# Optimization experiments

Hardware: AMD Instinct MI355X
Metric: run time of the kernel (lower is better)

Reference implementation:

```python
import jax, jax.numpy as jnp
import numpy as np

N_NODES = 100000
N_EDGES = 1600000
IN_FEATS = 256
OUT_FEATS = 128


def setup_inputs() -> dict:
    key = jax.random.key(0)
    k1, k2, k3, k4 = jax.random.split(key, 4)
    feat = jax.random.normal(k1, (N_NODES, IN_FEATS), dtype=jnp.float32)
    # Glorot-uniform-like weight
    limit = np.sqrt(6.0 / (IN_FEATS + OUT_FEATS)).astype(np.float32)
    weight = jax.random.uniform(k2, (IN_FEATS, OUT_FEATS), dtype=jnp.float32,
                                minval=-limit, maxval=limit)
    bias = jnp.zeros((OUT_FEATS,), dtype=jnp.float32)
    src = jax.random.randint(k3, (N_EDGES,), 0, N_NODES, dtype=jnp.int32)
    dst = jax.random.randint(k4, (N_EDGES,), 0, N_NODES, dtype=jnp.int32)
    return {"feat": feat, "weight": weight, "bias": bias, "src": src, "dst": dst}


def reference(feat, weight, bias, src, dst):
    n = feat.shape[0]
    # in-degree per node (edges point src -> dst), clipped to >= 1
    deg = jax.ops.segment_sum(jnp.ones_like(dst, dtype=feat.dtype), dst,
                              num_segments=n)
    norm = jnp.clip(deg, 1.0, None) ** -0.5          # [N]
    norm = norm[:, None]                             # [N, 1]
    h = feat * norm                                  # src-side normalization
    # in_feats > out_feats: project first, then aggregate (cheaper messages)
    h = h @ weight                                   # [N, out]
    agg = jax.ops.segment_sum(h[src], dst, num_segments=n)  # sparse sum-aggregate
    rst = agg * norm + bias                          # dst-side norm + bias
    return rst
```

## Files before the change

kernel.cpp:

```cpp
#include <hip/hip_runtime.h>
#include <hip/hip_bf16.h>

#define IN_F 256
#define OUT_F 128
#define BSH 7
#define BNODES 128
#define MAXBUCK 1024
#define BIN1A_BLOCKS 256
#define BIN1B_BLOCKS 256
#define GEMM_BLOCKS 256
#define BM 32

typedef short bf16x8 __attribute__((ext_vector_type(8)));
typedef float f32x4 __attribute__((ext_vector_type(4)));
typedef unsigned short us8 __attribute__((ext_vector_type(8)));

__device__ __forceinline__ unsigned short f2bf(float x) {
    union { __hip_bfloat16 b; unsigned short u; } cv;
    cv.b = __float2bfloat16(x);
    return cv.u;
}
__device__ inline float bf2f(unsigned short x) {
    union { unsigned u; float f; } v; v.u = ((unsigned)x) << 16;
    return v.f;
}

__device__ __forceinline__ void gload_lds16(const void* g, void* l) {
    __builtin_amdgcn_global_load_lds(
        (const __attribute__((address_space(1))) unsigned int*)g,
        (__attribute__((address_space(3))) unsigned int*)l,
        16, 0, 0);
}

__global__ __launch_bounds__(256) void prep_kernel(const float* __restrict__ W,
                                                   unsigned short* __restrict__ Wt,
                                                   const int* __restrict__ dst,
                                                   int* __restrict__ bhist,
                                                   int* __restrict__ perbhist,
                                                   int n_edges, int nbuck) {
    if ((int)blockIdx.x < BIN1A_BLOCKS) {
        __shared__ int hist[MAXBUCK];
        const int tid = threadIdx.x;
        const int chunk = (n_edges + BIN1A_BLOCKS - 1) / BIN1A_BLOCKS;
        const int lo = blockIdx.x * chunk;
        const int hi = min(lo + chunk, n_edges);

        for (int i = tid; i < MAXBUCK; i += 256) hist[i] = 0;
        __syncthreads();
        for (int e = lo + tid; e < hi; e += 256)
            atomicAdd(&hist[dst[e] >> BSH], 1);
        __syncthreads();
        int* myrow = perbhist + (size_t)blockIdx.x * MAXBUCK;
        for (int i = tid; i < nbuck; i += 256) {
            int c = hist[i];
            myrow[i] = c;
            if (c) atomicAdd(&bhist[i], c);
        }
    } else {
        int n = blockIdx.x - BIN1A_BLOCKS;
        int k = threadIdx.x;
        Wt[n * IN_F + k] = f2bf(W[k * OUT_F + n]);
    }
}

__global__ __launch_bounds__(1024) void bin1b_kernel(const int* __restrict__ src,
                                                     const int* __restrict__ dst,
                                                     const int* __restrict__ bhist,
                                                     const int* __restrict__ perbhist,
                                                     int* __restrict__ gcur0,
                                                     unsigned* __restrict__ ebuf,
                                                     int n_edges, int nbuck) {
    __shared__ int scanv[MAXBUCK];
    __shared__ int hist[MAXBUCK];
    __shared__ int lbase[MAXBUCK];
    const int tid = threadIdx.x;
    const int chunk = (n_edges + BIN1B_BLOCKS - 1) / BIN1B_BLOCKS;
    const int lo = blockIdx.x * chunk;
    const int hi = min(lo + chunk, n_edges);

    int own = (tid < nbuck) ? bhist[tid] : 0;
    scanv[tid] = own;
    __syncthreads();
    #pragma unroll
    for (int off = 1; off < MAXBUCK; off <<= 1) {
        int t = (tid >= off) ? scanv[tid - off] : 0;
        __syncthreads();
        scanv[tid] += t;
        __syncthreads();
    }
    int bstart_t = scanv[tid] - own;
    __syncthreads();
    scanv[tid] = bstart_t;
    __syncthreads();

    if (tid < nbuck) {
        int c = perbhist[(size_t)blockIdx.x * MAXBUCK + tid];
        lbase[tid] = (c > 0) ? (scanv[tid] + atomicAdd(&gcur0[tid], c)) : 0;
        hist[tid] = 0;
    }
    __syncthreads();
    for (int e = lo + tid; e < hi; e += 1024) {
        int d = dst[e];
        int bkt = d >> BSH;
        int off = atomicAdd(&hist[bkt], 1);
        ebuf[lbase[bkt] + off] = ((unsigned)src[e] << BSH) | (unsigned)(d & (BNODES - 1));
    }
}

__global__ __launch_bounds__(1024) void gemm_mfma(const float* __restrict__ feat,
                                                  const unsigned short* __restrict__ Wt,
                                                  unsigned short* __restrict__ h,
                                                  int n_nodes) {
    __shared__ float As[3][BM * IN_F];

    const int tid  = threadIdx.x;
    const int wave = tid >> 6;
    const int lane = tid & 63;
    const int q    = lane >> 4;
    const int rr   = lane & 15;
    const int rowgrp = wave & 1;
    const int colgrp = wave >> 1;

    const int ntiles = (n_nodes + BM - 1) / BM;
    const int nit = ((int)blockIdx.x < ntiles)
                  ? ((ntiles - (int)blockIdx.x + GEMM_BLOCKS - 1) / GEMM_BLOCKS) : 0;

    const int brow = colgrp * 16 + rr;

    bf16x8 bq[8];
    #pragma unroll
    for (int k0 = 0; k0 < 8; ++k0)
        bq[k0] = *reinterpret_cast<const bf16x8*>(
            Wt + (size_t)brow * IN_F + (k0 * 4 + q) * 8);

    #pragma unroll
    for (int pb = 0; pb < 2; ++pb) {
        if (pb < nit) {
            const int R0 = ((int)blockIdx.x + pb * GEMM_BLOCKS) * BM;
            #pragma unroll
            for (int ii = 0; ii < 2; ++ii) {
                int r  = ii * 16 + wave;
                int rg = R0 + r; if (rg >= n_nodes) rg = n_nodes - 1;
                gload_lds16(feat + (size_t)rg * IN_F + ((lane ^ (r & 7)) * 4),
                            &As[pb][r * IN_F]);
            }
        }
    }

    const int arow = rowgrp * 16 + rr;

    int t = (int)blockIdx.x;
    for (int i = 0; i < nit; ++i, t += GEMM_BLOCKS) {
        if (nit < 4)          asm volatile("s_waitcnt vmcnt(0)" ::: "memory");
        else if (i == 0)      asm volatile("s_waitcnt vmcnt(2)" ::: "memory");
        else if (i == 1)      asm volatile("s_waitcnt vmcnt(6)" ::: "memory");
        else if (i < nit - 1) asm volatile("s_waitcnt vmcnt(10)" ::: "memory");
        else                  asm volatile("s_waitcnt vmcnt(8)" ::: "memory");
        __builtin_amdgcn_s_barrier();

        if (i + 2 < nit) {
            const int R0n = (t + 2 * GEMM_BLOCKS) * BM;
            float* dbuf = As[(i + 2) % 3];
            #pragma unroll
            for (int ii = 0; ii < 2; ++ii) {
                int r  = ii * 16 + wave;
                int rg = R0n + r; if (rg >= n_nodes) rg = n_nodes - 1;
                gload_lds16(feat + (size_t)rg * IN_F + ((lane ^ (r & 7)) * 4),
                            &dbuf[r * IN_F]);
            }
        }

        f32x4 acc = (f32x4){0.f, 0.f, 0.f, 0.f};
        const f32x4* ap = reinterpret_cast<const f32x4*>(&As[i % 3][arow * IN_F]);
        #pragma unroll
        for (int k0 = 0; k0 < 8; ++k0) {
            f32x4 a0 = ap[(k0 * 8 + 2 * q)     ^ (rr & 7)];
            f32x4 a1 = ap[(k0 * 8 + 2 * q + 1) ^ (rr & 7)];
            bf16x8 afr;
            afr[0] = (short)f2bf(a0[0]);
            afr[1] = (short)f2bf(a0[1]);
            afr[2] = (short)f2bf(a0[2]);
            afr[3] = (short)f2bf(a0[3]);
            afr[4] = (short)f2bf(a1[0]);
            afr[5] = (short)f2bf(a1[1]);
            afr[6] = (short)f2bf(a1[2]);
            afr[7] = (short)f2bf(a1[3]);
            acc = __builtin_amdgcn_mfma_f32_16x16x32_bf16(afr, bq[k0], acc, 0, 0, 0);
        }

        const int orow0 = t * BM + rowgrp * 16 + q * 4;
        const int col   = colgrp * 16 + rr;
        #pragma unroll
        for (int j = 0; j < 4; ++j)
            h[(size_t)(orow0 + j) * OUT_F + col] = f2bf(acc[j]);
    }
}

__global__ __launch_bounds__(256) void bin2_kernel(const unsigned* __restrict__ ebuf,
                                                   const int* __restrict__ bhist,
                                                   int* __restrict__ rstart,
                                                   float* __restrict__ norm,
                                                   int* __restrict__ eidx,
                                                   int n_nodes, int nbuck) {
    __shared__ int bs[MAXBUCK];
    __shared__ int lcnt[BNODES];
    __shared__ int lex[BNODES];
    __shared__ int sh[256];
    const int tid = threadIdx.x;
    const int node0 = blockIdx.x << BSH;

    {
        int v[4], s = 0;
        #pragma unroll
        for (int j = 0; j < 4; ++j) {
            int idx = tid * 4 + j;
            v[j] = (idx < nbuck) ? bhist[idx] : 0;
            s += v[j];
        }
        sh[tid] = s;
        __syncthreads();
        #pragma unroll
        for (int off = 1; off < 256; off <<= 1) {
            int t = (tid >= off) ? sh[tid - off] : 0;
            __syncthreads();
            sh[tid] += t;
            __syncthreads();
        }
        int ex = sh[tid] - s;
        #pragma unroll
        for (int j = 0; j < 4; ++j) {
            bs[tid * 4 + j] = ex;
            ex += v[j];
        }
    }
    __syncthreads();

    const int e0 = bs[blockIdx.x];
    const int e1 = e0 + bhist[blockIdx.x];

    if (tid < BNODES) lcnt[tid] = 0;
    __syncthreads();
    for (int e = e0 + tid; e < e1; e += 256)
        atomicAdd(&lcnt[ebuf[e] & (BNODES - 1)], 1);
    __syncthreads();

    int own = (tid < BNODES) ? lcnt[tid] : 0;
    if (tid < BNODES) lex[tid] = own;
    __syncthreads();
    #pragma unroll
    for (int off = 1; off < BNODES; off <<= 1) {
        int t = (tid >= off && tid < BNODES) ? lex[tid - off] : 0;
        __syncthreads();
        if (tid < BNODES) lex[tid] += t;
        __syncthreads();
    }
    if (tid < BNODES) {
        int ex = lex[tid] - own;
        lex[tid] = ex;
        int g = node0 + tid;
        if (g <= n_nodes) rstart[g] = e0 + ex;
        if (g < n_nodes) {
            float d = (float)own;
            if (d < 1.0f) d = 1.0f;
            norm[g] = 1.0f / sqrtf(d);
        }
        lcnt[tid] = 0;
    }
    __syncthreads();

    for (int e = e0 + tid; e < e1; e += 256) {
        unsigned pk = ebuf[e];
        int dl = pk & (BNODES - 1);
        int pos = atomicAdd(&lcnt[dl], 1);
        eidx[e0 + lex[dl] + pos] = (int)(pk >> BSH);
    }
}

__global__ __launch_bounds__(256) void agg_kernel(const unsigned short* __restrict__ h,
                                                  const int* __restrict__ eidx,
                                                  const int* __restrict__ rstart,
                                                  const float* __restrict__ norm,
                                                  const float* __restrict__ bias,
                                                  float* __restrict__ out,
                                                  int n_nodes) {
    const int wave = threadIdx.x >> 6;
    const int lane = threadIdx.x & 63;
    const int grp  = lane >> 4;
    const int gl   = lane & 15;
    const int node = blockIdx.x * 4 + wave;
    if (node >= n_nodes) return;

    const int start = rstart[node];
    const int cnt   = rstart[node + 1] - start;
    const unsigned short* __restrict__ hb = h + gl * 8;

    float acc[8] = {0.f, 0.f, 0.f, 0.f, 0.f, 0.f, 0.f, 0.f};

    for (int base = 0; base < cnt; base += 64) {
        const int rem = min(64, cnt - base);
        int   ev = (lane < rem) ? eidx[start + base + lane] : 0;
        float nv = (lane < rem) ? norm[ev] : 0.f;

        int j = 0;
        for (; j + 16 <= rem; j += 16) {
            int   s0 = __shfl(ev, j + grp);
            int   s1 = __shfl(ev, j + grp + 4);
            int   s2 = __shfl(ev, j + grp + 8);
            int   s3 = __shfl(ev, j + grp + 12);
            float n0 = __shfl(nv, j + grp);
            float n1 = __shfl(nv, j + grp + 4);
            float n2 = __shfl(nv, j + grp + 8);
            float n3 = __shfl(nv, j + grp + 12);
            us8 v0 = *reinterpret_cast<const us8*>(hb + (size_t)s0 * OUT_F);
            us8 v1 = *reinterpret_cast<const us8*>(hb + (size_t)s1 * OUT_F);
            us8 v2 = *reinterpret_cast<const us8*>(hb + (size_t)s2 * OUT_F);
            us8 v3 = *reinterpret_cast<const us8*>(hb + (size_t)s3 * OUT_F);
            #pragma unroll
            for (int qq = 0; qq < 8; ++qq) {
                acc[qq] += bf2f(v0[qq]) * n0 + bf2f(v1[qq]) * n1
                         + bf2f(v2[qq]) * n2 + bf2f(v3[qq]) * n3;
            }
        }
        for (; j < rem; j += 4) {
            int   je = j + grp;
            int   jc = min(je, rem - 1);
            int   s  = __shfl(ev, jc);
            float nm = __shfl(nv, jc);
            if (je >= rem) nm = 0.f;
            us8 v = *reinterpret_cast<const us8*>(hb + (size_t)s * OUT_F);
            #pragma unroll
            for (int qq = 0; qq < 8; ++qq)
                acc[qq] += bf2f(v[qq]) * nm;
        }
    }

    #pragma unroll
    for (int qq = 0; qq < 8; ++qq) {
        acc[qq] += __shfl_xor(acc[qq], 16);
        acc[qq] += __shfl_xor(acc[qq], 32);
    }

    if (grp == 0) {
        const float nd = norm[node];
        const float4 b0 = *reinterpret_cast<const float4*>(bias + gl * 8);
        const float4 b1 = *reinterpret_cast<const float4*>(bias + gl * 8 + 4);
        float4 r0, r1;
        r0.x = acc[0] * nd + b0.x;
        r0.y = acc[1] * nd + b0.y;
        r0.z = acc[2] * nd + b0.z;
        r0.w = acc[3] * nd + b0.w;
        r1.x = acc[4] * nd + b1.x;
        r1.y = acc[5] * nd + b1.y;
        r1.z = acc[6] * nd + b1.z;
        r1.w = acc[7] * nd + b1.w;
        float* o = out + (size_t)node * OUT_F + gl * 8;
        *reinterpret_cast<float4*>(o)     = r0;
        *reinterpret_cast<float4*>(o + 4) = r1;
    }
}

extern "C" void kernel_launch(void* const* d_in, const int* in_sizes, int n_in,
                              void* d_out, int out_size, void* d_ws, size_t ws_size,
                              hipStream_t stream) {
    const float* feat   = (const float*)d_in[0];
    const float* weight = (const float*)d_in[1];
    const float* bias   = (const float*)d_in[2];
    const int*   src    = (const int*)d_in[3];
    const int*   dst    = (const int*)d_in[4];
    float* out = (float*)d_out;

    const int n_nodes = in_sizes[0] / IN_F;
    const int n_edges = in_sizes[3];
    const int nbuck   = (n_nodes + BNODES - 1) >> BSH;

    char* ws = (char*)d_ws;
    size_t off = 0;
    auto alloc = [&](size_t bytes) {
        char* p = ws + off;
        off += (bytes + 15) & ~(size_t)15;
        return p;
    };
    unsigned short* h  = (unsigned short*)alloc((size_t)(n_nodes + BM) * OUT_F * 2);
    float* norm        = (float*)alloc((size_t)n_nodes * 4);
    int*   rstart      = (int*)alloc(((size_t)n_nodes + 1) * 4);
    int*   bhist       = (int*)alloc(2 * MAXBUCK * 4);
    int*   gcur0       = bhist + MAXBUCK;
    int*   perbhist    = (int*)alloc((size_t)BIN1A_BLOCKS * MAXBUCK * 4);
    unsigned short* Wt = (unsigned short*)alloc((size_t)OUT_F * IN_F * 2);
    unsigned* ebuf     = (unsigned*)alloc((size_t)n_edges * 4);
    int*   eidx        = (int*)alloc((size_t)n_edges * 4);

    hipMemsetAsync(bhist, 0, 2 * MAXBUCK * sizeof(int), stream);
    prep_kernel<<<BIN1A_BLOCKS + OUT_F, 256, 0, stream>>>(weight, Wt, dst, bhist,
                                                          perbhist, n_edges, nbuck);
    gemm_mfma<<<GEMM_BLOCKS, 1024, 0, stream>>>(feat, Wt, h, n_nodes);
    bin1b_kernel<<<BIN1B_BLOCKS, 1024, 0, stream>>>(src, dst, bhist, perbhist,
                                                    gcur0, ebuf, n_edges, nbuck);
    bin2_kernel<<<nbuck, 256, 0, stream>>>(ebuf, bhist, rstart, norm, eidx,
                                           n_nodes, nbuck);
    agg_kernel<<<(n_nodes + 3) / 4, 256, 0, stream>>>(h, eidx, rstart, norm, bias, out, n_nodes);
}
```

Measured before the change: 144.7 us.

## Merge GEMM and edge binning into one launch with double-buffered GEMM

Combines the bf16 MFMA projection kernel and the second edge-binning pass into one heterogeneous launch, where the first blocks do binning and the rest do GEMM, so the two independent stages can run at the same time on the GPU. It drops one kernel launch and lets memory-bound scatter work share the machine with the GEMM. The GEMM pipeline goes from a triple-buffered LDS scheme with hand-tuned vmcnt waits to a double buffer with __syncthreads, because the shared 64KB LDS allocation only fits two tiles. This may expose more load latency per tile, and the large static LDS now also applies to the binning blocks, limiting how many blocks fit per CU.

```diff
diff --git a/kernel.cpp b/kernel.cpp
--- a/kernel.cpp
+++ b/kernel.cpp
@@ -63,136 +63,130 @@
     }
 }
 
-__global__ __launch_bounds__(1024) void bin1b_kernel(const int* __restrict__ src,
-                                                     const int* __restrict__ dst,
-                                                     const int* __restrict__ bhist,
-                                                     const int* __restrict__ perbhist,
-                                                     int* __restrict__ gcur0,
-                                                     unsigned* __restrict__ ebuf,
-                                                     int n_edges, int nbuck) {
-    __shared__ int scanv[MAXBUCK];
-    __shared__ int hist[MAXBUCK];
-    __shared__ int lbase[MAXBUCK];
-    const int tid = threadIdx.x;
-    const int chunk = (n_edges + BIN1B_BLOCKS - 1) / BIN1B_BLOCKS;
-    const int lo = blockIdx.x * chunk;
-    const int hi = min(lo + chunk, n_edges);
-
-    int own = (tid < nbuck) ? bhist[tid] : 0;
-    scanv[tid] = own;
-    __syncthreads();
-    #pragma unroll
-    for (int off = 1; off < MAXBUCK; off <<= 1) {
-        int t = (tid >= off) ? scanv[tid - off] : 0;
-        __syncthreads();
-        scanv[tid] += t;
-        __syncthreads();
-    }
-    int bstart_t = scanv[tid] - own;
-    __syncthreads();
-    scanv[tid] = bstart_t;
-    __syncthreads();
-
-    if (tid < nbuck) {
-        int c = perbhist[(size_t)blockIdx.x * MAXBUCK + tid];
-        lbase[tid] = (c > 0) ? (scanv[tid] + atomicAdd(&gcur0[tid], c)) : 0;
-        hist[tid] = 0;
-    }
-    __syncthreads();
-    for (int e = lo + tid; e < hi; e += 1024) {
-        int d = dst[e];
-        int bkt = d >> BSH;
-        int off = atomicAdd(&hist[bkt], 1);
-        ebuf[lbase[bkt] + off] = ((unsigned)src[e] << BSH) | (unsigned)(d & (BNODES - 1));
-    }
-}
-
-__global__ __launch_bounds__(1024) void gemm_mfma(const float* __restrict__ feat,
-                                                  const unsigned short* __restrict__ Wt,
-                                                  unsigned short* __restrict__ h,
-                                                  int n_nodes) {
-    __shared__ float As[3][BM * IN_F];
-
-    const int tid  = threadIdx.x;
-    const int wave = tid >> 6;
-    const int lane = tid & 63;
-    const int q    = lane >> 4;
-    const int rr   = lane & 15;
-    const int rowgrp = wave & 1;
-    const int colgrp = wave >> 1;
-
-    const int ntiles = (n_nodes + BM - 1) / BM;
-    const int nit = ((int)blockIdx.x < ntiles)
-                  ? ((ntiles - (int)blockIdx.x + GEMM_BLOCKS - 1) / GEMM_BLOCKS) : 0;
-
-    const int brow = colgrp * 16 + rr;
-
-    bf16x8 bq[8];
-    #pragma unroll
-    for (int k0 = 0; k0 < 8; ++k0)
-        bq[k0] = *reinterpret_cast<const bf16x8*>(
-            Wt + (size_t)brow * IN_F + (k0 * 4 + q) * 8);
-
-    #pragma unroll
-    for (int pb = 0; pb < 2; ++pb) {
-        if (pb < nit) {
-            const int R0 = ((int)blockIdx.x + pb * GEMM_BLOCKS) * BM;
+__global__ __launch_bounds__(1024, 8) void gemm_bin_kernel(
+        const float* __restrict__ feat, const unsigned short* __restrict__ Wt,
+        unsigned short* __restrict__ h, int n_nodes,
+        const int* __restrict__ src, const int* __restrict__ dst,
+        const int* __restrict__ bhist, const int* __restrict__ perbhist,
+        int* __restrict__ gcur0, unsigned* __restrict__ ebuf,
+        int n_edges, int nbuck) {
+
+    __shared__ __align__(16) char smem[65536];
+
+    if ((int)blockIdx.x < BIN1B_BLOCKS) {
+        int* scanv = (int*)smem;
+        int* hist  = scanv + MAXBUCK;
+        int* lbase = hist + MAXBUCK;
+        const int tid = threadIdx.x;
+        const int chunk = (n_edges + BIN1B_BLOCKS - 1) / BIN1B_BLOCKS;
+        const int lo = blockIdx.x * chunk;
+        const int hi = min(lo + chunk, n_edges);
+
+        int own = (tid < nbuck) ? bhist[tid] : 0;
+        scanv[tid] = own;
+        __syncthreads();
+        #pragma unroll
+        for (int off = 1; off < MAXBUCK; off <<= 1) {
+            int t = (tid >= off) ? scanv[tid - off] : 0;
+            __syncthreads();
+            scanv[tid] += t;
+            __syncthreads();
+        }
+        int bstart_t = scanv[tid] - own;
+        __syncthreads();
+        scanv[tid] = bstart_t;
+        __syncthreads();
+
+        if (tid < nbuck) {
+            int c = perbhist[(size_t)blockIdx.x * MAXBUCK + tid];
+            lbase[tid] = (c > 0) ? (scanv[tid] + atomicAdd(&gcur0[tid], c)) : 0;
+            hist[tid] = 0;
+        }
+        __syncthreads();
+        for (int e = lo + tid; e < hi; e += 1024) {
+            int d = dst[e];
+            int bkt = d >> BSH;
+            int off = atomicAdd(&hist[bkt], 1);
+            ebuf[lbase[bkt] + off] = ((unsigned)src[e] << BSH) | (unsigned)(d & (BNODES - 1));
+        }
+    } else {
+        float (*As)[BM * IN_F] = (float (*)[BM * IN_F])smem;
+
+        const int tid  = threadIdx.x;
+        const int wave = tid >> 6;
+        const int lane = tid & 63;
+        const int q    = lane >> 4;
+        const int rr   = lane & 15;
+        const int rowgrp = wave & 1;
+        const int colgrp = wave >> 1;
+        const int gb   = (int)blockIdx.x - BIN1B_BLOCKS;
+
+        const int ntiles = (n_nodes + BM - 1) / BM;
+        const int nit = (gb < ntiles)
+                      ? ((ntiles - gb + GEMM_BLOCKS - 1) / GEMM_BLOCKS) : 0;
+
+        const int brow = colgrp * 16 + rr;
+
+        bf16x8 bq[8];
+        #pragma unroll
+        for (int k0 = 0; k0 < 8; ++k0)
+            bq[k0] = *reinterpret_cast<const bf16x8*>(
+                Wt + (size_t)brow * IN_F + (k0 * 4 + q) * 8);
+
+        if (0 < nit) {
+            const int R0 = gb * BM;
             #pragma unroll
             for (int ii = 0; ii < 2; ++ii) {
                 int r  = ii * 16 + wave;
                 int rg = R0 + r; if (rg >= n_nodes) rg = n_nodes - 1;
                 gload_lds16(feat + (size_t)rg * IN_F + ((lane ^ (r & 7)) * 4),
-                            &As[pb][r * IN_F]);
+                            &As[0][r * IN_F]);
             }
         }
-    }
-
-    const int arow = rowgrp * 16 + rr;
-
-    int t = (int)blockIdx.x;
-    for (int i = 0; i < nit; ++i, t += GEMM_BLOCKS) {
-        if (nit < 4)          asm volatile("s_waitcnt vmcnt(0)" ::: "memory");
-        else if (i == 0)      asm volatile("s_waitcnt vmcnt(2)" ::: "memory");
-        else if (i == 1)      asm volatile("s_waitcnt vmcnt(6)" ::: "memory");
-        else if (i < nit - 1) asm volatile("s_waitcnt vmcnt(10)" ::: "memory");
-        else                  asm volatile("s_waitcnt vmcnt(8)" ::: "memory");
-        __builtin_amdgcn_s_barrier();
-
-        if (i + 2 < nit) {
-            const int R0n = (t + 2 * GEMM_BLOCKS) * BM;
-            float* dbuf = As[(i + 2) % 3];
-            #pragma unroll
-            for (int ii = 0; ii < 2; ++ii) {
-                int r  = ii * 16 + wave;
-                int rg = R0n + r; if (rg >= n_nodes) rg = n_nodes - 1;
-                gload_lds16(feat + (size_t)rg * IN_F + ((lane ^ (r & 7)) * 4),
-                            &dbuf[r * IN_F]);
+        __syncthreads();
+
+        const int arow = rowgrp * 16 + rr;
+
+        int t = gb, buf = 0;
+        for (int i = 0; i < nit; ++i, t += GEMM_BLOCKS) {
+            if (i + 1 < nit) {
+                const int R0n = (t + GEMM_BLOCKS) * BM;
+                #pragma unroll
+                for (int ii = 0; ii < 2; ++ii) {
+                    int r  = ii * 16 + wave;
+                    int rg = R0n + r; if (rg >= n_nodes) rg = n_nodes - 1;
+                    gload_lds16(feat + (size_t)rg * IN_F + ((lane ^ (r & 7)) * 4),
+                                &As[buf ^ 1][r * IN_F]);
+                }
             }
-        }
-
-        f32x4 acc = (f32x4){0.f, 0.f, 0.f, 0.f};
-        const f32x4* ap = reinterpret_cast<const f32x4*>(&As[i % 3][arow * IN_F]);
-        #pragma unroll
-        for (int k0 = 0; k0 < 8; ++k0) {
-            f32x4 a0 = ap[(k0 * 8 + 2 * q)     ^ (rr & 7)];
-            f32x4 a1 = ap[(k0 * 8 + 2 * q + 1) ^ (rr & 7)];
-            bf16x8 afr;
-            afr[0] = (short)f2bf(a0[0]);
-            afr[1] = (short)f2bf(a0[1]);
-            afr[2] = (short)f2bf(a0[2]);
-            afr[3] = (short)f2bf(a0[3]);
-            afr[4] = (short)f2bf(a1[0]);
-            afr[5] = (short)f2bf(a1[1]);
-            afr[6] = (short)f2bf(a1[2]);
-            afr[7] = (short)f2bf(a1[3]);
-            acc = __builtin_amdgcn_mfma_f32_16x16x32_bf16(afr, bq[k0], acc, 0, 0, 0);
-        }
-
-        const int orow0 = t * BM + rowgrp * 16 + q * 4;
-        const int col   = colgrp * 16 + rr;
-        #pragma unroll
-        for (int j = 0; j < 4; ++j)
-            h[(size_t)(orow0 + j) * OUT_F + col] = f2bf(acc[j]);
+
+            f32x4 acc = (f32x4){0.f, 0.f, 0.f, 0.f};
+            const f32x4* ap = reinterpret_cast<const f32x4*>(&As[buf][arow * IN_F]);
+            #pragma unroll
+            for (int k0 = 0; k0 < 8; ++k0) {
+                f32x4 a0 = ap[(k0 * 8 + 2 * q)     ^ (rr & 7)];
+                f32x4 a1 = ap[(k0 * 8 + 2 * q + 1) ^ (rr & 7)];
+                bf16x8 afr;
+                afr[0] = (short)f2bf(a0[0]);
+                afr[1] = (short)f2bf(a0[1]);
+                afr[2] = (short)f2bf(a0[2]);
+                afr[3] = (short)f2bf(a0[3]);
+                afr[4] = (short)f2bf(a1[0]);
+                afr[5] = (short)f2bf(a1[1]);
+                afr[6] = (short)f2bf(a1[2]);
+                afr[7] = (short)f2bf(a1[3]);
+                acc = __builtin_amdgcn_mfma_f32_16x16x32_bf16(afr, bq[k0], acc, 0, 0, 0);
+            }
+
+            __syncthreads();
+
+            const int orow0 = t * BM + rowgrp * 16 + q * 4;
+            const int col   = colgrp * 16 + rr;
+            #pragma unroll
+            for (int j = 0; j < 4; ++j)
+                h[(size_t)(orow0 + j) * OUT_F + col] = f2bf(acc[j]);
+            buf ^= 1;
+        }
     }
 }
 
@@ -393,9 +387,9 @@
     hipMemsetAsync(bhist, 0, 2 * MAXBUCK * sizeof(int), stream);
     prep_kernel<<<BIN1A_BLOCKS + OUT_F, 256, 0, stream>>>(weight, Wt, dst, bhist,
                                                           perbhist, n_edges, nbuck);
-    gemm_mfma<<<GEMM_BLOCKS, 1024, 0, stream>>>(feat, Wt, h, n_nodes);
-    bin1b_kernel<<<BIN1B_BLOCKS, 1024, 0, stream>>>(src, dst, bhist, perbhist,
-                                                    gcur0, ebuf, n_edges, nbuck);
+    gemm_bin_kernel<<<BIN1B_BLOCKS + GEMM_BLOCKS, 1024, 0, stream>>>(
+        feat, Wt, h, n_nodes, src, dst, bhist, perbhist, gcur0, ebuf,
+        n_edges, nbuck);
     bin2_kernel<<<nbuck, 256, 0, stream>>>(ebuf, bhist, rstart, norm, eidx,
                                            n_nodes, nbuck);
     agg_kernel<<<(n_nodes + 3) / 4, 256, 0, stream>>>(h, eidx, rstart, norm, bias, out, n_nodes);
```

Measured after the change: 151.7 us. 4.8% more time.

## Enlarge GEMM row tile and reuse A fragments across two column MFMAs

Applied to the files above, without the earlier changes.

Doubles the GEMM row tile from 32 to 64. Each wave now computes two 16-column output tiles from one converted bf16 A fragment, which halves the LDS reads and fp32-to-bf16 conversions per output. The triple-buffered prefetch with hand-tuned vmcnt waits becomes a simpler double buffer synchronised by __syncthreads, which gives a shallower prefetch pipeline and adds a full barrier every iteration. LDS use grows to 128 KB. Since 100000 is not a multiple of 64, the last tile writes rows past n_nodes into h, which is only safe if h is padded.

```diff
diff --git a/kernel.cpp b/kernel.cpp
--- a/kernel.cpp
+++ b/kernel.cpp
@@ -9,7 +9,7 @@
 #define BIN1A_BLOCKS 256
 #define BIN1B_BLOCKS 256
 #define GEMM_BLOCKS 256
-#define BM 32
+#define BM 64
 
 typedef short bf16x8 __attribute__((ext_vector_type(8)));
 typedef float f32x4 __attribute__((ext_vector_type(4)));
@@ -111,67 +111,62 @@
                                                   const unsigned short* __restrict__ Wt,
                                                   unsigned short* __restrict__ h,
                                                   int n_nodes) {
-    __shared__ float As[3][BM * IN_F];
+    __shared__ float As[2][BM * IN_F];
 
     const int tid  = threadIdx.x;
     const int wave = tid >> 6;
     const int lane = tid & 63;
     const int q    = lane >> 4;
     const int rr   = lane & 15;
-    const int rowgrp = wave & 1;
-    const int colgrp = wave >> 1;
+    const int rowgrp  = wave & 3;
+    const int colpair = wave >> 2;
 
     const int ntiles = (n_nodes + BM - 1) / BM;
     const int nit = ((int)blockIdx.x < ntiles)
                   ? ((ntiles - (int)blockIdx.x + GEMM_BLOCKS - 1) / GEMM_BLOCKS) : 0;
 
-    const int brow = colgrp * 16 + rr;
-
-    bf16x8 bq[8];
+    const int brow0 = colpair * 32 + rr;
+    const int brow1 = colpair * 32 + 16 + rr;
+
+    bf16x8 bq0[8], bq1[8];
     #pragma unroll
-    for (int k0 = 0; k0 < 8; ++k0)
-        bq[k0] = *reinterpret_cast<const bf16x8*>(
-            Wt + (size_t)brow * IN_F + (k0 * 4 + q) * 8);
-
-    #pragma unroll
-    for (int pb = 0; pb < 2; ++pb) {
-        if (pb < nit) {
-            const int R0 = ((int)blockIdx.x + pb * GEMM_BLOCKS) * BM;
+    for (int k0 = 0; k0 < 8; ++k0) {
+        bq0[k0] = *reinterpret_cast<const bf16x8*>(
+            Wt + (size_t)brow0 * IN_F + (k0 * 4 + q) * 8);
+        bq1[k0] = *reinterpret_cast<const bf16x8*>(
+            Wt + (size_t)brow1 * IN_F + (k0 * 4 + q) * 8);
+    }
+
+    if (0 < nit) {
+        const int R0 = (int)blockIdx.x * BM;
+        #pragma unroll
+        for (int ii = 0; ii < 4; ++ii) {
+            int r  = ii * 16 + wave;
+            int rg = R0 + r; if (rg >= n_nodes) rg = n_nodes - 1;
+            gload_lds16(feat + (size_t)rg * IN_F + ((lane ^ (r & 7)) * 4),
+                        &As[0][r * IN_F]);
+        }
+    }
+    __syncthreads();
+
+    const int arow = rowgrp * 16 + rr;
+
+    int t = (int)blockIdx.x, buf = 0;
+    for (int i = 0; i < nit; ++i, t += GEMM_BLOCKS) {
+        if (i + 1 < nit) {
+            const int R0n = (t + GEMM_BLOCKS) * BM;
             #pragma unroll
-            for (int ii = 0; ii < 2; ++ii) {
-                int r  = ii * 16 + wave;
-                int rg = R0 + r; if (rg >= n_nodes) rg = n_nodes - 1;
-                gload_lds16(feat + (size_t)rg * IN_F + ((lane ^ (r & 7)) * 4),
-                            &As[pb][r * IN_F]);
-            }
-        }
-    }
-
-    const int arow = rowgrp * 16 + rr;
-
-    int t = (int)blockIdx.x;
-    for (int i = 0; i < nit; ++i, t += GEMM_BLOCKS) {
-        if (nit < 4)          asm volatile("s_waitcnt vmcnt(0)" ::: "memory");
-        else if (i == 0)      asm volatile("s_waitcnt vmcnt(2)" ::: "memory");
-        else if (i == 1)      asm volatile("s_waitcnt vmcnt(6)" ::: "memory");
-        else if (i < nit - 1) asm volatile("s_waitcnt vmcnt(10)" ::: "memory");
-        else                  asm volatile("s_waitcnt vmcnt(8)" ::: "memory");
-        __builtin_amdgcn_s_barrier();
-
-        if (i + 2 < nit) {
-            const int R0n = (t + 2 * GEMM_BLOCKS) * BM;
-            float* dbuf = As[(i + 2) % 3];
-            #pragma unroll
-            for (int ii = 0; ii < 2; ++ii) {
+            for (int ii = 0; ii < 4; ++ii) {
                 int r  = ii * 16 + wave;
                 int rg = R0n + r; if (rg >= n_nodes) rg = n_nodes - 1;
                 gload_lds16(feat + (size_t)rg * IN_F + ((lane ^ (r & 7)) * 4),
-                            &dbuf[r * IN_F]);
+                            &As[buf ^ 1][r * IN_F]);
             }
         }
 
-        f32x4 acc = (f32x4){0.f, 0.f, 0.f, 0.f};
-        const f32x4* ap = reinterpret_cast<const f32x4*>(&As[i % 3][arow * IN_F]);
+        f32x4 acc0 = (f32x4){0.f, 0.f, 0.f, 0.f};
+        f32x4 acc1 = (f32x4){0.f, 0.f, 0.f, 0.f};
+        const f32x4* ap = reinterpret_cast<const f32x4*>(&As[buf][arow * IN_F]);
         #pragma unroll
         for (int k0 = 0; k0 < 8; ++k0) {
             f32x4 a0 = ap[(k0 * 8 + 2 * q)     ^ (rr & 7)];
@@ -185,14 +180,21 @@
             afr[5] = (short)f2bf(a1[1]);
             afr[6] = (short)f2bf(a1[2]);
             afr[7] = (short)f2bf(a1[3]);
-            acc = __builtin_amdgcn_mfma_f32_16x16x32_bf16(afr, bq[k0], acc, 0, 0, 0);
-        }
+            acc0 = __builtin_amdgcn_mfma_f32_16x16x32_bf16(afr, bq0[k0], acc0, 0, 0, 0);
+            acc1 = __builtin_amdgcn_mfma_f32_16x16x32_bf16(afr, bq1[k0], acc1, 0, 0, 0);
+        }
+
+        __syncthreads();
 
         const int orow0 = t * BM + rowgrp * 16 + q * 4;
-        const int col   = colgrp * 16 + rr;
-        #pragma unroll
-        for (int j = 0; j < 4; ++j)
-            h[(size_t)(orow0 + j) * OUT_F + col] = f2bf(acc[j]);
+        const int col0  = colpair * 32 + rr;
+        const int col1  = colpair * 32 + 16 + rr;
+        #pragma unroll
+        for (int j = 0; j < 4; ++j) {
+            h[(size_t)(orow0 + j) * OUT_F + col0] = f2bf(acc0[j]);
+            h[(size_t)(orow0 + j) * OUT_F + col1] = f2bf(acc1[j]);
+        }
+        buf ^= 1;
     }
 }
 
```

After: 146.8 us. Within noise of the previous version (+1.4%).
